# Performance work log

Hardware: AMD Instinct MI355X
Metric: run time of the kernel (lower is better)

The kernel has to match this reference:

```python
import jax, jax.numpy as jnp
import numpy as np

K_FACTOR = 8
TOP_N = 4
NUM_LAYER = 2


def setup_inputs() -> dict:
    key = jax.random.key(0)
    ks = jax.random.split(key, 5)
    num_ent, num_rel, n_edges = 50000, 500, 500000
    emb_dim = 128
    emb_s = emb_dim // K_FACTOR  # 16
    ent_embeddings = jax.random.normal(ks[0], (num_ent, emb_dim), jnp.float32)
    rel_embeddings = jax.random.normal(ks[1], (num_rel, TOP_N * emb_s), jnp.float32)
    rel_att = jax.random.normal(ks[2], (num_rel, K_FACTOR), jnp.float32)
    edge_index = jax.random.randint(ks[3], (2, n_edges), 0, num_ent)
    edge_type = jax.random.randint(ks[4], (n_edges,), 0, num_rel)
    return dict(ent_embeddings=ent_embeddings, rel_embeddings=rel_embeddings,
                rel_att=rel_att, edge_index=edge_index, edge_type=edge_type,
                num_ent=num_ent, num_rel=num_rel)


def _segment_mean(src, idx, n):
    s = jax.ops.segment_sum(src, idx, num_segments=n)
    c = jax.ops.segment_sum(jnp.ones((src.shape[0],), src.dtype), idx, num_segments=n)
    return jnp.where(c[:, None] > 0, s / jnp.maximum(c, 1.0)[:, None], 0.0)


def _conv(x, r, r_att, ei, et, num_ent, num_rel):
    emb_dim = x.shape[1]
    s = emb_dim // K_FACTOR
    # add self-loop edges with relation id num_rel (zero embedding / zero att)
    loop = jnp.arange(num_ent, dtype=ei.dtype)
    ei = jnp.concatenate([ei, jnp.stack([loop, loop])], axis=1)
    et = jnp.concatenate([et, jnp.full((num_ent,), num_rel, et.dtype)])
    r_pad = jnp.concatenate([r, jnp.zeros((1, r.shape[1]), r.dtype)], axis=0)
    ra_pad = jnp.concatenate([r_att, jnp.zeros((1, K_FACTOR), r_att.dtype)], axis=0)

    neigh_t = x[ei[1]]          # (E, D)
    neigh_h = x[ei[0]]          # (E, D)
    neigh_r = r_pad[et]         # (E, top_n*s)
    att = jax.nn.softmax(ra_pad[et], axis=1)      # (E, k)
    order = jnp.argsort(-att, axis=-1)             # descending sort indices
    top, rem = order[:, :TOP_N], order[:, TOP_N:]

    E = neigh_h.shape[0]
    tf = neigh_t.reshape(E, K_FACTOR, s)
    hf = neigh_h.reshape(E, K_FACTOR, s)
    t_top = jnp.take_along_axis(tf, top[:, :, None], axis=1)  # (E, top_n, s)
    h_top = jnp.take_along_axis(hf, top[:, :, None], axis=1)
    h_rem = jnp.take_along_axis(hf, rem[:, :, None], axis=1)

    tmp = (h_top.reshape(E, -1) + neigh_r).reshape(E, TOP_N, s)
    rows = jnp.arange(E)[:, None]
    # the fresh random ent_embed in the original is fully overwritten by the
    # two scatters (top + remaining cover all k_factor slots) -> deterministic
    ent = (jnp.zeros((E, K_FACTOR, s), x.dtype)
           .at[rows, top].set(tmp)
           .at[rows, rem].set(h_rem))

    ent_embed = _segment_mean(ent.reshape(E, emb_dim), ei[1], num_ent)
    rel_embed = _segment_mean(t_top.reshape(E, -1) - h_top.reshape(E, -1), et, num_rel + 1)
    return jax.nn.relu(ent_embed), rel_embed[:-1], r_att


def reference(ent_embeddings, rel_embeddings, rel_att, edge_index, edge_type, num_ent, num_rel):
    x, r = ent_embeddings, rel_embeddings
    for _ in range(NUM_LAYER):
        # faithful to MAE.forward: the ORIGINAL rel_att is passed to every layer
        x, r, _ = _conv(x, r, rel_att, edge_index, edge_type, num_ent, num_rel)
    return (x, r)
```

## Files before the change

kernel.cpp:

```cpp
#include <hip/hip_runtime.h>

#define KF 8
#define TN 4
#define SDIM 16
#define EMB 128
#define NS 8
#define NB 128
#define NT 512
#define NRMAX 512
#define SCE 1024

typedef unsigned int u32;

__device__ __forceinline__ u32 pack2bf(float a, float b) {
    u32 ua = __float_as_uint(a), ub = __float_as_uint(b);
    ua = (ua + 0x7FFFu + ((ua >> 16) & 1u)) >> 16;
    ub = (ub + 0x7FFFu + ((ub >> 16) & 1u)) >> 16;
    return ua | (ub << 16);
}
__device__ __forceinline__ float lo16(u32 w) { return __uint_as_float(w << 16); }
__device__ __forceinline__ float hi16(u32 w) { return __uint_as_float(w & 0xFFFF0000u); }

__global__ __launch_bounds__(256) void k_init(int* __restrict__ deg, int num_ent,
                                              int* __restrict__ rcnt, int num_rel,
                                              float* __restrict__ rsumA, float* __restrict__ rsumB,
                                              int nrsum, int* __restrict__ flags, int nblk) {
    int i = blockIdx.x * 256 + threadIdx.x;
    if (i < num_ent) deg[i] = 0;
    if (i < num_rel) rcnt[i] = 0;
    if (i < nrsum) { rsumA[i] = 0.f; rsumB[i] = 0.f; }
    if (i < nblk) flags[i] = 0;
}

__global__ __launch_bounds__(256) void k_hist(const int* __restrict__ tails, const int* __restrict__ types,
                                              int nE, int num_rel,
                                              int* __restrict__ deg, int* __restrict__ rcnt) {
    __shared__ int hist[NRMAX];
    for (int q = threadIdx.x; q < num_rel; q += 256) hist[q] = 0;
    __syncthreads();
    for (int i = blockIdx.x * 256 + threadIdx.x; i < nE; i += gridDim.x * 256) {
        atomicAdd(&deg[tails[i]], 1);
        atomicAdd(&hist[types[i]], 1);
    }
    __syncthreads();
    for (int q = threadIdx.x; q < num_rel; q += 256) {
        int h = hist[q];
        if (h) atomicAdd(&rcnt[q], h);
    }
}

__device__ void scan_small(const int* __restrict__ in, int* __restrict__ out, int* __restrict__ out2, int n) {
    __shared__ int warp_sums[16];
    int carry = 0;
    int lane = threadIdx.x & 63, wid = threadIdx.x >> 6;
    int nw = blockDim.x >> 6;
    for (int base = 0; base < n; base += blockDim.x) {
        int i = base + (int)threadIdx.x;
        int v = (i < n) ? in[i] : 0;
        int sv = v;
        for (int o = 1; o < 64; o <<= 1) { int t = __shfl_up(sv, o, 64); if (lane >= o) sv += t; }
        if (lane == 63) warp_sums[wid] = sv;
        __syncthreads();
        if (wid == 0 && lane < nw) {
            int ws = warp_sums[lane];
            for (int o = 1; o < 16; o <<= 1) { int t = __shfl_up(ws, o, 64); if (lane >= o) ws += t; }
            warp_sums[lane] = ws;
        }
        __syncthreads();
        int wofs = (wid > 0) ? warp_sums[wid - 1] : 0;
        int total = warp_sums[nw - 1];
        if (i < n) {
            int e = carry + wofs + sv - v;
            out[i] = e;
            if (out2) out2[i] = e;
        }
        carry += total;
        __syncthreads();
    }
    if (threadIdx.x == 0) out[n] = carry;
}

__global__ __launch_bounds__(256) void k_scan_fused(const int* __restrict__ deg,
                                                    int* __restrict__ tail_off, int* __restrict__ tail_cur,
                                                    int n, int nblk,
                                                    int* __restrict__ vals, int* __restrict__ flags,
                                                    const int* __restrict__ rcnt, int* __restrict__ rel_off,
                                                    int* __restrict__ rel_cur, int num_rel) {
    int b = blockIdx.x;
    if (b == nblk) { scan_small(rcnt, rel_off, rel_cur, num_rel); return; }
    __shared__ int wsum[4];
    __shared__ int pw[4];
    __shared__ int sprefix;
    int tid = threadIdx.x;
    int lane = tid & 63, wid = tid >> 6;
    int i0 = b * SCE + tid * 4;
    int v[4];
#pragma unroll
    for (int j = 0; j < 4; ++j) { int i = i0 + j; v[j] = (i < n) ? deg[i] : 0; }
    int tsum = v[0] + v[1] + v[2] + v[3];
    int sv = tsum;
    for (int o = 1; o < 64; o <<= 1) { int t = __shfl_up(sv, o, 64); if (lane >= o) sv += t; }
    if (lane == 63) wsum[wid] = sv;
    __syncthreads();
    if (tid == 0) {
        int s = 0;
        for (int w = 0; w < 4; ++w) { int t = wsum[w]; wsum[w] = s; s += t; }
        vals[b] = s;
        __threadfence();
        atomicExch(&flags[b], 1);
    }
    __syncthreads();
    int p = 0;
    for (int i = tid; i < b; i += 256) {
        while (atomicAdd(&flags[i], 0) == 0) {}
        p += atomicAdd(&vals[i], 0);
    }
    for (int o = 1; o < 64; o <<= 1) p += __shfl_xor(p, o, 64);
    if (lane == 0) pw[wid] = p;
    __syncthreads();
    if (tid == 0) sprefix = pw[0] + pw[1] + pw[2] + pw[3];
    __syncthreads();
    int run = sprefix + wsum[wid] + (sv - tsum);
#pragma unroll
    for (int j = 0; j < 4; ++j) {
        int i = i0 + j;
        if (i < n) { tail_off[i] = run; tail_cur[i] = run; }
        run += v[j];
    }
    if (b == nblk - 1 && tid == 0) tail_off[n] = sprefix + vals[b];
}

__global__ __launch_bounds__(256) void k_scatter_fused(
        const int* __restrict__ heads, const int* __restrict__ tails, const int* __restrict__ types,
        int nE, int num_ent, int num_rel,
        int* __restrict__ tail_cur, u32* __restrict__ tail_edges,
        int* __restrict__ rel_cur, u32* __restrict__ rel_edges,
        const float4* __restrict__ x4, u32* __restrict__ xh, int n4,
        const float* __restrict__ rel_att, const float* __restrict__ r0,
        int* __restrict__ posmap, int* __restrict__ topmap, u32* __restrict__ pr0,
        int nc, int np) {
    int bid = blockIdx.x;
    if (bid < NT) {
        for (int i = bid * 256 + (int)threadIdx.x; i < nE; i += NT * 256) {
            int t = tails[i];
            int p = atomicAdd(&tail_cur[t], 1);
            tail_edges[p] = (u32)heads[i] | ((u32)types[i] << 16);
        }
    } else if (bid < NT + NB) {
        __shared__ int hist[NRMAX];
        __shared__ int base[NRMAX];
        int bi = bid - NT;
        int c = (bi & 7) * (NB >> 3) + (bi >> 3);
        int chunk = (nE + NB - 1) / NB;
        int beg = c * chunk, end = min(beg + chunk, nE);
        for (int q = threadIdx.x; q < num_rel; q += 256) hist[q] = 0;
        __syncthreads();
        for (int i = beg + (int)threadIdx.x; i < end; i += 256) atomicAdd(&hist[types[i]], 1);
        __syncthreads();
        for (int q = threadIdx.x; q < num_rel; q += 256) {
            int h = hist[q];
            base[q] = h > 0 ? atomicAdd(&rel_cur[q], h) : 0;
            hist[q] = 0;
        }
        __syncthreads();
        for (int i = beg + (int)threadIdx.x; i < end; i += 256) {
            int q = types[i];
            int rank = atomicAdd(&hist[q], 1);
            rel_edges[base[q] + rank] = (u32)tails[i] | ((u32)heads[i] << 16);
        }
    } else if (bid < NT + NB + nc) {
        int i = (bid - NT - NB) * 256 + (int)threadIdx.x;
        if (i < n4) {
            float4 v = x4[i];
            ((uint2*)xh)[i] = make_uint2(pack2bf(v.x, v.y), pack2bf(v.z, v.w));
        }
    } else {
        int q = (bid - NT - NB - nc) * 4 + ((int)threadIdx.x >> 6);
        if (q >= num_rel) return;
        int i = threadIdx.x & 63;
        float v[KF]; int idx[KF];
        for (int k = 0; k < KF; ++k) { v[k] = rel_att[q * KF + k]; idx[k] = k; }
        for (int a = 1; a < KF; ++a) {
            float va = v[a]; int ia = idx[a]; int j = a - 1;
            while (j >= 0 && v[j] < va) { v[j + 1] = v[j]; idx[j + 1] = idx[j]; --j; }
            v[j + 1] = va; idx[j + 1] = ia;
        }
        int pos[KF];
        for (int k = 0; k < KF; ++k) pos[k] = -1;
        for (int j = 0; j < TN; ++j) pos[idx[j]] = j;
        if (i < KF) posmap[q * KF + i] = pos[i];
        if (i < TN) topmap[q * TN + i] = idx[i];
        int k = i >> 3;
        int p = pos[k];
        u32 w = 0;
        if (p >= 0) {
            float a = r0[q * 64 + p * SDIM + ((2 * i) & 15)];
            float b = r0[q * 64 + p * SDIM + ((2 * i + 1) & 15)];
            w = pack2bf(a, b);
        }
        pr0[q * 64 + i] = w;
    }
}

__global__ __launch_bounds__(256) void k_rel_pass(const u32* __restrict__ xh,
                                                  const int* __restrict__ rel_off,
                                                  const u32* __restrict__ rel_edges,
                                                  const int* __restrict__ topmap,
                                                  float* __restrict__ rsum_top) {
    int bid = blockIdx.x;
    int q = bid >> 3, s = bid & 7;
    int lane = threadIdx.x & 63;
    int qw = lane >> 4, c = lane & 15;
    int wid = threadIdx.x >> 6;
    int k = topmap[q * TN + (c >> 2)];
    int woff = k * 8 + (c & 3) * 2;
    int beg = rel_off[q], end = rel_off[q + 1];
    float acc[4] = {0.f, 0.f, 0.f, 0.f};
    for (int e = beg + s * 16 + wid * 4 + qw; e < end; e += 128) {
        u32 ew = rel_edges[e];
        int t = (int)(ew & 0xFFFFu);
        int h = (int)(ew >> 16);
        uint2 ta = *(const uint2*)(xh + ((size_t)t << 6) + woff);
        uint2 hb = *(const uint2*)(xh + ((size_t)h << 6) + woff);
        acc[0] += lo16(ta.x) - lo16(hb.x);
        acc[1] += hi16(ta.x) - hi16(hb.x);
        acc[2] += lo16(ta.y) - lo16(hb.y);
        acc[3] += hi16(ta.y) - hi16(hb.y);
    }
#pragma unroll
    for (int d = 0; d < 4; ++d) {
        acc[d] += __shfl_xor(acc[d], 16, 64);
        acc[d] += __shfl_xor(acc[d], 32, 64);
    }
    __shared__ float prt[4][64];
    if (qw == 0) {
#pragma unroll
        for (int d = 0; d < 4; ++d) prt[wid][c * 4 + d] = acc[d];
    }
    __syncthreads();
    int tid = threadIdx.x;
    if (tid < 64) {
        float v = prt[0][tid] + prt[1][tid] + prt[2][tid] + prt[3][tid];
        atomicAdd(&rsum_top[(size_t)q * 64 + tid], v);
    }
}

template <bool OUT_BF16>
__global__ __launch_bounds__(256) void k_ent_pass(const u32* __restrict__ xh, const u32* __restrict__ prh,
                                                  const int* __restrict__ tail_off,
                                                  const u32* __restrict__ tail_edges,
                                                  u32* __restrict__ xout_h, float4* __restrict__ xout_f,
                                                  int num_ent, int egrid,
                                                  const float* __restrict__ rsum_top,
                                                  const int* __restrict__ rel_off,
                                                  const int* __restrict__ posmap,
                                                  u32* __restrict__ pr_out, float* __restrict__ rout,
                                                  int num_rel) {
    int bid = blockIdx.x;
    if (bid >= egrid) {
        if (OUT_BF16) {
            int q = (bid - egrid) * 4 + ((int)threadIdx.x >> 6);
            if (q >= num_rel) return;
            int i = threadIdx.x & 63;
            int k = i >> 3;
            int pos = posmap[q * KF + k];
            int cnt = rel_off[q + 1] - rel_off[q];
            u32 w = 0;
            if (pos >= 0 && cnt > 0) {
                float inv = 1.f / (float)cnt;
                int d0 = (2 * i) & 15;
                float a = rsum_top[(size_t)q * 64 + pos * SDIM + d0] * inv;
                float b = rsum_top[(size_t)q * 64 + pos * SDIM + d0 + 1] * inv;
                w = pack2bf(a, b);
            }
            pr_out[q * 64 + i] = w;
        } else {
            int idx = (bid - egrid) * 256 + (int)threadIdx.x;
            if (idx < num_rel * 64) {
                int q = idx >> 6;
                int cnt = rel_off[q + 1] - rel_off[q];
                rout[idx] = cnt > 0 ? rsum_top[idx] / (float)cnt : 0.f;
            }
        }
        return;
    }
    int wid = threadIdx.x >> 6;
    int t = bid * 4 + wid;
    if (t >= num_ent) return;
    int lane = threadIdx.x & 63;
    int qw = lane >> 4, c = lane & 15;
    int beg = tail_off[t], end = tail_off[t + 1];
    int deg = end - beg;
    float acc[8] = {0.f, 0.f, 0.f, 0.f, 0.f, 0.f, 0.f, 0.f};
    for (int b2 = 0; b2 < deg; b2 += 64) {
        int m = min(64, deg - b2);
        u32 ew = (lane < m) ? tail_edges[beg + b2 + lane] : 0u;
        for (int j = 0; j < m; j += 4) {
            int idx = j + qw;
            u32 w = __shfl(ew, idx, 64);
            uint4 xr = make_uint4(0, 0, 0, 0), pr = make_uint4(0, 0, 0, 0);
            if (idx < m) {
                int h = (int)(w & 0xFFFFu);
                int q = (int)(w >> 16);
                xr = *(const uint4*)(xh + ((size_t)h << 6) + (c << 2));
                pr = *(const uint4*)(prh + ((size_t)q << 6) + (c << 2));
            }
            acc[0] += lo16(xr.x) + lo16(pr.x);
            acc[1] += hi16(xr.x) + hi16(pr.x);
            acc[2] += lo16(xr.y) + lo16(pr.y);
            acc[3] += hi16(xr.y) + hi16(pr.y);
            acc[4] += lo16(xr.z) + lo16(pr.z);
            acc[5] += hi16(xr.z) + hi16(pr.z);
            acc[6] += lo16(xr.w) + lo16(pr.w);
            acc[7] += hi16(xr.w) + hi16(pr.w);
        }
    }
#pragma unroll
    for (int d = 0; d < 8; ++d) {
        acc[d] += __shfl_xor(acc[d], 16, 64);
        acc[d] += __shfl_xor(acc[d], 32, 64);
    }
    if (qw == 0) {
        uint4 sw = *(const uint4*)(xh + ((size_t)t << 6) + (c << 2));
        float s[8] = { lo16(sw.x), hi16(sw.x), lo16(sw.y), hi16(sw.y),
                       lo16(sw.z), hi16(sw.z), lo16(sw.w), hi16(sw.w) };
        float inv = 1.f / (float)(deg + 1);
        float o[8];
#pragma unroll
        for (int d = 0; d < 8; ++d) {
            float v = (acc[d] + s[d]) * inv;
            o[d] = v > 0.f ? v : 0.f;
        }
        if (OUT_BF16) {
            uint4 ow = make_uint4(pack2bf(o[0], o[1]), pack2bf(o[2], o[3]),
                                  pack2bf(o[4], o[5]), pack2bf(o[6], o[7]));
            *(uint4*)(xout_h + ((size_t)t << 6) + (c << 2)) = ow;
        } else {
            xout_f[((size_t)t << 5) + (c << 1)]     = make_float4(o[0], o[1], o[2], o[3]);
            xout_f[((size_t)t << 5) + (c << 1) + 1] = make_float4(o[4], o[5], o[6], o[7]);
        }
    }
}

extern "C" void kernel_launch(void* const* d_in, const int* in_sizes, int n_in,
                              void* d_out, int out_size, void* d_ws, size_t ws_size,
                              hipStream_t stream) {
    const float* x0 = (const float*)d_in[0];
    const float* r0 = (const float*)d_in[1];
    const float* rel_att = (const float*)d_in[2];
    const int* edge_index = (const int*)d_in[3];
    const int* edge_type = (const int*)d_in[4];

    const int num_ent = in_sizes[0] / EMB;
    const int num_rel = in_sizes[2] / KF;
    const int nE = in_sizes[4];

    const int* heads = edge_index;
    const int* tails = edge_index + nE;

    const int nblk = (num_ent + SCE - 1) / SCE;
    const int n4 = num_ent * 32;
    const int nc = (n4 + 255) / 256;
    const int np = (num_rel + 3) / 4;

    char* base = (char*)d_ws;
    size_t off = 0;
    auto carve = [&](size_t bytes) { char* p = base + off; off = (off + bytes + 255) & ~(size_t)255; return p; };
    int* deg        = (int*)carve((size_t)num_ent * 4);
    int* tail_off   = (int*)carve((size_t)(num_ent + 1) * 4);
    int* tail_cur   = (int*)carve((size_t)num_ent * 4);
    u32* tail_edges = (u32*)carve((size_t)nE * 4);
    int* rcnt       = (int*)carve((size_t)num_rel * 4);
    int* rel_off    = (int*)carve((size_t)(num_rel + 1) * 4);
    int* rel_cur    = (int*)carve((size_t)num_rel * 4);
    u32* rel_edges  = (u32*)carve((size_t)nE * 4);
    int* posmap     = (int*)carve((size_t)num_rel * KF * 4);
    int* topmap     = (int*)carve((size_t)num_rel * TN * 4);
    int* svals      = (int*)carve((size_t)nblk * 4);
    int* sflags     = (int*)carve((size_t)nblk * 4);
    u32* x0h        = (u32*)carve((size_t)num_ent * EMB * 2);
    u32* x1h        = (u32*)carve((size_t)num_ent * EMB * 2);
    u32* pr0        = (u32*)carve((size_t)num_rel * 64 * 4);
    u32* pr1        = (u32*)carve((size_t)num_rel * 64 * 4);
    float* rsumA    = (float*)carve((size_t)num_rel * 64 * 4);
    float* rsumB    = (float*)carve((size_t)num_rel * 64 * 4);
    (void)ws_size;

    float* x_out = (float*)d_out;
    float* r_out = (float*)d_out + (size_t)num_ent * EMB;

    int initmax = num_ent > num_rel * 64 ? num_ent : num_rel * 64;
    k_init<<<(initmax + 255) / 256, 256, 0, stream>>>(deg, num_ent, rcnt, num_rel,
                                                      rsumA, rsumB, num_rel * 64, sflags, nblk);
    k_hist<<<512, 256, 0, stream>>>(tails, edge_type, nE, num_rel, deg, rcnt);
    k_scan_fused<<<nblk + 1, 256, 0, stream>>>(deg, tail_off, tail_cur, num_ent, nblk,
                                               svals, sflags, rcnt, rel_off, rel_cur, num_rel);
    k_scatter_fused<<<NT + NB + nc + np, 256, 0, stream>>>(
        heads, tails, edge_type, nE, num_ent, num_rel,
        tail_cur, tail_edges, rel_cur, rel_edges,
        (const float4*)x0, x0h, n4, rel_att, r0, posmap, topmap, pr0, nc, np);

    int egrid = (num_ent + 3) / 4;
    int nfin1 = (num_rel + 3) / 4;
    int nfin2 = (num_rel * 64 + 255) / 256;

    k_rel_pass<<<num_rel * NS, 256, 0, stream>>>(x0h, rel_off, rel_edges, topmap, rsumA);
    k_ent_pass<true><<<egrid + nfin1, 256, 0, stream>>>(x0h, pr0, tail_off, tail_edges,
                                                        x1h, nullptr, num_ent, egrid,
                                                        rsumA, rel_off, posmap, pr1, nullptr, num_rel);
    k_rel_pass<<<num_rel * NS, 256, 0, stream>>>(x1h, rel_off, rel_edges, topmap, rsumB);
    k_ent_pass<false><<<egrid + nfin2, 256, 0, stream>>>(x1h, pr1, tail_off, tail_edges,
                                                         nullptr, (float4*)x_out, num_ent, egrid,
                                                         rsumB, rel_off, nullptr, nullptr, r_out, num_rel);
}
```

Baseline: 200.9 us.

## Pre-bucket edges by tail range in histogram pass to localize CSR scatter

```diff
diff --git a/kernel.cpp b/kernel.cpp
--- a/kernel.cpp
+++ b/kernel.cpp
@@ -7,10 +7,12 @@
 #define NS 8
 #define NB 128
 #define NT 512
+#define NCHK 512
 #define NRMAX 512
 #define SCE 1024
 
 typedef unsigned int u32;
+typedef unsigned long long u64;
 
 __device__ __forceinline__ u32 pack2bf(float a, float b) {
     u32 ua = __float_as_uint(a), ub = __float_as_uint(b);
@@ -32,21 +34,36 @@
     if (i < nblk) flags[i] = 0;
 }
 
-__global__ __launch_bounds__(256) void k_hist(const int* __restrict__ tails, const int* __restrict__ types,
-                                              int nE, int num_rel,
-                                              int* __restrict__ deg, int* __restrict__ rcnt) {
+__global__ __launch_bounds__(256) void k_hist(const int* __restrict__ heads,
+                                              const int* __restrict__ tails,
+                                              const int* __restrict__ types,
+                                              int nE, int num_rel, int per, int C,
+                                              int* __restrict__ deg, int* __restrict__ rcnt,
+                                              u64* __restrict__ bucket, int* __restrict__ bcnt) {
     __shared__ int hist[NRMAX];
+    __shared__ int lcnt[8];
+    int blk = blockIdx.x;
     for (int q = threadIdx.x; q < num_rel; q += 256) hist[q] = 0;
-    __syncthreads();
-    for (int i = blockIdx.x * 256 + threadIdx.x; i < nE; i += gridDim.x * 256) {
-        atomicAdd(&deg[tails[i]], 1);
-        atomicAdd(&hist[types[i]], 1);
+    if (threadIdx.x < 8) lcnt[threadIdx.x] = 0;
+    __syncthreads();
+    int beg = blk * C, end = min(beg + C, nE);
+    size_t bkcap = (size_t)NCHK * C;
+    size_t chunkbase = (size_t)blk * C;
+    for (int i = beg + (int)threadIdx.x; i < end; i += 256) {
+        int t = tails[i], h = heads[i], q = types[i];
+        atomicAdd(&deg[t], 1);
+        atomicAdd(&hist[q], 1);
+        int bk = t / per;
+        int rank = atomicAdd(&lcnt[bk], 1);
+        bucket[(size_t)bk * bkcap + chunkbase + rank] =
+            (u64)(u32)t | ((u64)(u32)h << 16) | ((u64)(u32)q << 32);
     }
     __syncthreads();
     for (int q = threadIdx.x; q < num_rel; q += 256) {
         int h = hist[q];
         if (h) atomicAdd(&rcnt[q], h);
     }
+    if (threadIdx.x < 8) bcnt[blk * 8 + threadIdx.x] = lcnt[threadIdx.x];
 }
 
 __device__ void scan_small(const int* __restrict__ in, int* __restrict__ out, int* __restrict__ out2, int n) {
@@ -132,7 +149,8 @@
 
 __global__ __launch_bounds__(256) void k_scatter_fused(
         const int* __restrict__ heads, const int* __restrict__ tails, const int* __restrict__ types,
-        int nE, int num_ent, int num_rel,
+        int nE, int num_ent, int num_rel, int C,
+        const u64* __restrict__ bucket, const int* __restrict__ bcnt,
         int* __restrict__ tail_cur, u32* __restrict__ tail_edges,
         int* __restrict__ rel_cur, u32* __restrict__ rel_edges,
         const float4* __restrict__ x4, u32* __restrict__ xh, int n4,
@@ -141,10 +159,17 @@
         int nc, int np) {
     int bid = blockIdx.x;
     if (bid < NT) {
-        for (int i = bid * 256 + (int)threadIdx.x; i < nE; i += NT * 256) {
-            int t = tails[i];
-            int p = atomicAdd(&tail_cur[t], 1);
-            tail_edges[p] = (u32)heads[i] | ((u32)types[i] << 16);
+        int p = bid & 7, w = bid >> 3;
+        size_t bkcap = (size_t)NCHK * C;
+        for (int seg = w; seg < NCHK; seg += (NT >> 3)) {
+            int m = bcnt[seg * 8 + p];
+            size_t base = (size_t)p * bkcap + (size_t)seg * C;
+            for (int j = threadIdx.x; j < m; j += 256) {
+                u64 e = bucket[base + j];
+                int t = (int)(e & 0xFFFFull);
+                int pos = atomicAdd(&tail_cur[t], 1);
+                tail_edges[pos] = (u32)(e >> 16);
+            }
         }
     } else if (bid < NT + NB) {
         __shared__ int hist[NRMAX];
@@ -362,6 +387,8 @@
     const int n4 = num_ent * 32;
     const int nc = (n4 + 255) / 256;
     const int np = (num_rel + 3) / 4;
+    const int C = (nE + NCHK - 1) / NCHK;
+    const int per = (num_ent + 7) >> 3;
 
     char* base = (char*)d_ws;
     size_t off = 0;
@@ -378,6 +405,8 @@
     int* topmap     = (int*)carve((size_t)num_rel * TN * 4);
     int* svals      = (int*)carve((size_t)nblk * 4);
     int* sflags     = (int*)carve((size_t)nblk * 4);
+    u64* bucket     = (u64*)carve((size_t)8 * NCHK * C * 8);
+    int* bcnt       = (int*)carve((size_t)NCHK * 8 * 4);
     u32* x0h        = (u32*)carve((size_t)num_ent * EMB * 2);
     u32* x1h        = (u32*)carve((size_t)num_ent * EMB * 2);
     u32* pr0        = (u32*)carve((size_t)num_rel * 64 * 4);
@@ -392,11 +421,12 @@
     int initmax = num_ent > num_rel * 64 ? num_ent : num_rel * 64;
     k_init<<<(initmax + 255) / 256, 256, 0, stream>>>(deg, num_ent, rcnt, num_rel,
                                                       rsumA, rsumB, num_rel * 64, sflags, nblk);
-    k_hist<<<512, 256, 0, stream>>>(tails, edge_type, nE, num_rel, deg, rcnt);
+    k_hist<<<NCHK, 256, 0, stream>>>(heads, tails, edge_type, nE, num_rel, per, C,
+                                     deg, rcnt, bucket, bcnt);
     k_scan_fused<<<nblk + 1, 256, 0, stream>>>(deg, tail_off, tail_cur, num_ent, nblk,
                                                svals, sflags, rcnt, rel_off, rel_cur, num_rel);
     k_scatter_fused<<<NT + NB + nc + np, 256, 0, stream>>>(
-        heads, tails, edge_type, nE, num_ent, num_rel,
+        heads, tails, edge_type, nE, num_ent, num_rel, C, bucket, bcnt,
         tail_cur, tail_edges, rel_cur, rel_edges,
         (const float4*)x0, x0h, n4, rel_att, r0, posmap, topmap, pr0, nc, np);
 
```

After: 196.2 us. 1.02x faster.
